# Kernel optimization log

Measured on AMD Instinct MI355X. Metric: run time of the kernel, lower is better.

Reference implementation:

```python
import jax, jax.numpy as jnp
import numpy as np


def _mlp(x, w1, b1, w2, b2):
    # full_connected / full_connected_conv1d with channels [3,16,32]:
    # pointwise Linear -> LeakyReLU -> Linear (kernel-size-1 conv == linear on last dim)
    h = jax.nn.leaky_relu(x @ w1 + b1)
    return h @ w2 + b2


def setup_inputs() -> dict:
    key = jax.random.key(0)
    ks = jax.random.split(key, 10)
    P, K = 100000, 16            # points, neighbors per point
    C_IN, C_H, C_OUT, C_W = 3, 16, 32, 64
    center = jax.random.normal(ks[0], (P, 1, C_IN), dtype=jnp.float32)
    other = jax.random.normal(ks[1], (P, K, C_IN), dtype=jnp.float32)
    s1 = 1.0 / np.sqrt(C_IN)
    s2 = 1.0 / np.sqrt(C_H)
    # 6 stacked 3->16->32 MLPs: [q, center_k, center_v, other_k, other_v, pos]
    mlp_w1 = jax.random.normal(ks[2], (6, C_IN, C_H), dtype=jnp.float32) * s1
    mlp_b1 = jax.random.normal(ks[3], (6, C_H), dtype=jnp.float32) * s1
    mlp_w2 = jax.random.normal(ks[4], (6, C_H, C_OUT), dtype=jnp.float32) * s2
    mlp_b2 = jax.random.normal(ks[5], (6, C_OUT), dtype=jnp.float32) * s2
    # weight_process: 32->64->32
    wp_w1 = jax.random.normal(ks[6], (C_OUT, C_W), dtype=jnp.float32) / np.sqrt(C_OUT)
    wp_b1 = jax.random.normal(ks[7], (C_W,), dtype=jnp.float32) / np.sqrt(C_OUT)
    wp_w2 = jax.random.normal(ks[8], (C_W, C_OUT), dtype=jnp.float32) / np.sqrt(C_W)
    wp_b2 = jax.random.normal(ks[9], (C_OUT,), dtype=jnp.float32) / np.sqrt(C_W)
    return {"center": center, "other": other,
            "mlp_w1": mlp_w1, "mlp_b1": mlp_b1, "mlp_w2": mlp_w2, "mlp_b2": mlp_b2,
            "wp_w1": wp_w1, "wp_b1": wp_b1, "wp_w2": wp_w2, "wp_b2": wp_b2}


def reference(center, other, mlp_w1, mlp_b1, mlp_w2, mlp_b2, wp_w1, wp_b1, wp_w2, wp_b2):
    # center: [P,1,3], other: [P,K,3]
    q = _mlp(center, mlp_w1[0], mlp_b1[0], mlp_w2[0], mlp_b2[0])      # [P,1,32]
    ck = _mlp(center, mlp_w1[1], mlp_b1[1], mlp_w2[1], mlp_b2[1])     # [P,1,32]
    cv = _mlp(center, mlp_w1[2], mlp_b1[2], mlp_w2[2], mlp_b2[2])     # [P,1,32]
    ok = _mlp(other, mlp_w1[3], mlp_b1[3], mlp_w2[3], mlp_b2[3])      # [P,K,32]
    ov = _mlp(other, mlp_w1[4], mlp_b1[4], mlp_w2[4], mlp_b2[4])      # [P,K,32]
    k_all = jnp.concatenate([ck, ok], axis=-2)                        # [P,K+1,32]
    v_all = jnp.concatenate([cv, ov], axis=-2)                        # [P,K+1,32]
    fea_minus = center - jnp.concatenate([center, other], axis=-2)    # [P,K+1,3]
    pos = _mlp(fea_minus, mlp_w1[5], mlp_b1[5], mlp_w2[5], mlp_b2[5]) # [P,K+1,32]
    fea_weight = _mlp(q - k_all + pos, wp_w1, wp_b1, wp_w2, wp_b2)    # [P,K+1,32]
    # vector attention: softmax over CHANNEL dim (-1), weighted sum over neighbors (-2)
    attn = jax.nn.softmax(fea_weight, axis=-1) * (v_all + pos)
    return jnp.sum(attn, axis=-2)                                     # [P,32]
```

## Files before the change

### kernel.cpp

```cpp
#include <hip/hip_runtime.h>


constexpr int PPB = 15;
constexpr float LOG2E = 1.44269504088896340736f;

typedef __attribute__((ext_vector_type(8))) short bf8;
typedef __attribute__((ext_vector_type(4))) float f4;
typedef __attribute__((ext_vector_type(2))) float f2;
typedef __attribute__((ext_vector_type(2))) __bf16 bfp2;

__device__ __forceinline__ unsigned int pkbf(float a, float b) {
  f2 v; v[0] = a; v[1] = b;
  const bfp2 r = __builtin_convertvector(v, bfp2);
  return __builtin_bit_cast(unsigned int, r);
}
__device__ __forceinline__ unsigned short us16(float a) {
  return (unsigned short)((__builtin_bit_cast(unsigned int, a) + 0x8000u) >> 16);
}
__device__ __forceinline__ bf8 mkbf8(const f4& a, const f4& b) {
  uint4 u;
  u.x = pkbf(a[0], a[1]); u.y = pkbf(a[2], a[3]);
  u.z = pkbf(b[0], b[1]); u.w = pkbf(b[2], b[3]);
  return __builtin_bit_cast(bf8, u);
}
__device__ __forceinline__ f4 lrelu4(const f4& v) {
  return __builtin_elementwise_max(v, v * 0.01f);
}
__device__ __forceinline__ f2 lo2(const f4& v) { f2 r; r[0] = v[0]; r[1] = v[1]; return r; }
__device__ __forceinline__ f2 hi2(const f4& v) { f2 r; r[0] = v[2]; r[1] = v[3]; return r; }
__device__ __forceinline__ float exp2appx(float x) {
  const float t = __builtin_fmaf(x, 8388608.0f, 1064992232.0f);
  return __builtin_bit_cast(float, (int)t);
}
__device__ __forceinline__ f4 mfma32(bf8 a, bf8 b, f4 c) {
  return __builtin_amdgcn_mfma_f32_16x16x32_bf16(a, b, c, 0, 0, 0);
}

__device__ __forceinline__ int slotk(int q, int j) {
  return (j < 4) ? (q * 4 + j) : (16 + q * 4 + (j - 4));
}

__device__ __forceinline__ float w1v(const float* mw1, const float* mb1,
                                     int s, int k, int n) {
  const int cb = n >> 4, cc = n & 15;
  const int sk = s ? 1 : 3, sv = s ? 2 : 4;
  if (k < 3)  return cb == 0 ? mw1[sk * 48 + k * 16 + cc]
                   : (cb == 1 ? mw1[sv * 48 + k * 16 + cc] : 0.f);
  if (k < 6)  return cb == 2 ? mw1[5 * 48 + (k - 3) * 16 + cc] : 0.f;
  if (k < 9)  return cb == 3 ? mw1[0 * 48 + (k - 6) * 16 + cc] : 0.f;
  if (k == 9) {
    const int m = (cb == 0) ? sk : (cb == 1) ? sv : (cb == 2) ? 5 : 0;
    return mb1[m * 16 + cc];
  }
  return 0.f;
}
__device__ __forceinline__ float w2v(const float* mw2, int s, int k, int n) {
  const int sk = s ? 1 : 3, sv = s ? 2 : 4;
  if (n < 32) {
    if (k < 16)            return -mw2[sk * 512 + k * 32 + n];
    if (k >= 32 && k < 48) return  mw2[5 * 512 + (k - 32) * 32 + n];
    if (k >= 48)           return  mw2[0 * 512 + (k - 48) * 32 + n];
    return 0.f;
  } else {
    const int cc = n - 32;
    if (k >= 16 && k < 32) return mw2[sv * 512 + (k - 16) * 32 + cc];
    if (k >= 32 && k < 48) return mw2[5 * 512 + (k - 32) * 32 + cc];
    return 0.f;
  }
}

__global__ void prep_kernel(const float* __restrict__ mw1, const float* __restrict__ mb1,
                            const float* __restrict__ mw2, const float* __restrict__ mb2,
                            const float* __restrict__ ww1, const float* __restrict__ ww2,
                            unsigned short* __restrict__ ws16, float* __restrict__ wsf) {
  const int tid = blockIdx.x * 256 + threadIdx.x;
  const int lane = tid & 63, q = lane >> 4, l = lane & 15;
  if (tid < 2048) {
    const int f = tid >> 6;
    for (int j = 0; j < 8; j++) {
      float v;
      if (f < 8) {
        const int s = f >> 2, c = f & 3;
        v = w1v(mw1, mb1, s, q * 8 + j, c * 16 + l);
      } else if (f < 24) {
        const int g = f - 8, s = g >> 3, mc = (g >> 1) & 3, kc2 = g & 1;
        v = w2v(mw2, s, kc2 * 32 + slotk(q, j), mc * 16 + l);
      } else if (f < 28) {
        const int mc = f - 24;
        v = ww1[slotk(q, j) * 64 + mc * 16 + l];
      } else {
        const int g = f - 28, mc2 = g >> 1, kc2 = g & 1;
        v = ww2[(kc2 * 32 + slotk(q, j)) * 32 + mc2 * 16 + l] * LOG2E;
      }
      ws16[f * 512 + lane * 8 + j] = us16(v);
    }
  } else if (tid < 2176) {
    const int t2 = tid - 2048, grp = t2 >> 5, cc = t2 & 31;
    float v;
    if (grp == 0)      v = mb2[cc] - mb2[96 + cc] + mb2[160 + cc];
    else if (grp == 1) v = mb2[128 + cc] + mb2[160 + cc];
    else if (grp == 2) v = mb2[cc] - mb2[32 + cc] + mb2[160 + cc];
    else               v = mb2[64 + cc] + mb2[160 + cc];
    wsf[grp * 32 + cc] = v;
  }
}

__global__ __launch_bounds__(256, 2) void point_attn_kernel(
    const float* __restrict__ center, const float* __restrict__ other,
    const float* __restrict__ wb1, const float* __restrict__ wb2,
    const unsigned short* __restrict__ ws16, const float* __restrict__ wsf,
    float* __restrict__ out, int P) {
  __shared__ float pr[256 * 36];

  const int t = threadIdx.x, lane = t & 63, wv = t >> 6;
  const int q = lane >> 4, l = lane & 15;

  unsigned int d0, d1, d2, d3, d4;
  {
    const int isC = (t >= 240);
    const int pt = isC ? (t - 240) : (t >> 4);
    int p = blockIdx.x * PPB + pt;
    p = p < P ? p : P - 1;
    const float c0 = center[(size_t)p * 3 + 0];
    const float c1 = center[(size_t)p * 3 + 1];
    const float c2 = center[(size_t)p * 3 + 2];
    const float* op = other + ((size_t)p * 16 + (t & 15)) * 3;
    const float o0 = op[0], o1 = op[1], o2 = op[2];
    const float x0 = isC ? c0 : o0, x1 = isC ? c1 : o1, x2 = isC ? c2 : o2;
    const float g0 = c0 - x0, g1 = c1 - x1, g2 = c2 - x2;
    d0 = pkbf(x0, x1); d1 = pkbf(x2, g0); d2 = pkbf(g1, g2);
    d3 = pkbf(c0, c1); d4 = pkbf(c2, 1.0f);
  }

  bf8 W1[4], W2[4][2], P1[4], P2[2][2];
  f4 bw[2], bvp[2], b1f[4], b2f[2];

  auto loadSet = [&](int s) {
#pragma unroll
    for (int c = 0; c < 4; c++)
      W1[c] = *(const bf8*)(ws16 + ((s * 4 + c) * 512 + lane * 8));
#pragma unroll
    for (int mc = 0; mc < 4; mc++)
#pragma unroll
      for (int kc2 = 0; kc2 < 2; kc2++)
        W2[mc][kc2] = *(const bf8*)(ws16 + ((8 + s * 8 + mc * 2 + kc2) * 512 + lane * 8));
#pragma unroll
    for (int mc = 0; mc < 2; mc++) {
      bw[mc]  = *(const f4*)(wsf + s * 64 + mc * 16 + q * 4);
      bvp[mc] = *(const f4*)(wsf + s * 64 + 32 + mc * 16 + q * 4);
    }
  };

  loadSet(wv == 3 ? 1 : 0);
#pragma unroll
  for (int mc = 0; mc < 4; mc++)
    P1[mc] = *(const bf8*)(ws16 + ((24 + mc) * 512 + lane * 8));
#pragma unroll
  for (int mc2 = 0; mc2 < 2; mc2++)
#pragma unroll
    for (int kc2 = 0; kc2 < 2; kc2++)
      P2[mc2][kc2] = *(const bf8*)(ws16 + ((28 + mc2 * 2 + kc2) * 512 + lane * 8));
#pragma unroll
  for (int mc = 0; mc < 4; mc++) b1f[mc] = *(const f4*)(wb1 + mc * 16 + q * 4);
#pragma unroll
  for (int mc2 = 0; mc2 < 2; mc2++) {
    const f4 b = *(const f4*)(wb2 + mc2 * 16 + q * 4);
#pragma unroll
    for (int j = 0; j < 4; j++) b2f[mc2][j] = b[j] * LOG2E;
  }

  auto computeTile = [&](int T) {
    const int src = ((T & 3) << 4) | l;
    const unsigned int s0 = __shfl((int)d0, src), s1 = __shfl((int)d1, src),
                       s2 = __shfl((int)d2, src), s3 = __shfl((int)d3, src),
                       s4 = __shfl((int)d4, src);
    uint4 bu;
    bu.x = q == 0 ? s0 : (q == 1 ? s4 : 0u);
    bu.y = q == 0 ? s1 : 0u;
    bu.z = q == 0 ? s2 : 0u;
    bu.w = q == 0 ? s3 : 0u;
    const bf8 bx = __builtin_bit_cast(bf8, bu);
    const f4 fzero = {0.f, 0.f, 0.f, 0.f};

    f4 D1[4];
#pragma unroll
    for (int c = 0; c < 4; c++)
      D1[c] = lrelu4(mfma32(W1[c], bx, fzero));
    const bf8 hlo = mkbf8(D1[0], D1[1]);
    const bf8 hhi = mkbf8(D1[2], D1[3]);

    f4 wq[2], vpv[2];
#pragma unroll
    for (int mc = 0; mc < 4; mc++) {
      f4 acc = (mc < 2) ? bw[mc] : bvp[mc - 2];
      acc = mfma32(W2[mc][0], hlo, acc);
      acc = mfma32(W2[mc][1], hhi, acc);
      if (mc < 2) wq[mc] = acc; else vpv[mc - 2] = acc;
    }
    const bf8 wB = mkbf8(wq[0], wq[1]);

    f4 h2[4];
#pragma unroll
    for (int mc = 0; mc < 4; mc++)
      h2[mc] = lrelu4(mfma32(P1[mc], wB, b1f[mc]));
    const bf8 h2lo = mkbf8(h2[0], h2[1]);
    const bf8 h2hi = mkbf8(h2[2], h2[3]);

    f4 fw[2];
#pragma unroll
    for (int mc2 = 0; mc2 < 2; mc2++) {
      f4 acc = mfma32(P2[mc2][0], h2lo, b2f[mc2]);
      fw[mc2] = mfma32(P2[mc2][1], h2hi, acc);
    }

    f4 ex0, ex1;
#pragma unroll
    for (int j = 0; j < 4; j++) {
      ex0[j] = exp2appx(fw[0][j]);
      ex1[j] = exp2appx(fw[1][j]);
    }
    const f2 sA = lo2(ex0) + hi2(ex0);
    const f2 sB = lo2(ex1) + hi2(ex1);
    const f2 sC = sA + sB;
    float sum = sC[0] + sC[1];
    sum += __shfl_xor(sum, 16);
    sum += __shfl_xor(sum, 32);
    const float inv = __builtin_amdgcn_rcpf(sum);

    f4 iv; iv[0] = inv; iv[1] = inv; iv[2] = inv; iv[3] = inv;
    const f4 p0 = ex0 * iv * vpv[0];
    const f4 p1 = ex1 * iv * vpv[1];
    *(f4*)&pr[(T * 16 + l) * 36 + q * 4] = p0;
    *(f4*)&pr[(T * 16 + l) * 36 + 16 + q * 4] = p1;
  };

  computeTile(wv == 3 ? 15 : wv * 4);
  if (wv == 3) loadSet(0);
#pragma unroll
  for (int jj = 1; jj < 4; jj++)
    computeTile(wv == 3 ? (11 + jj) : (wv * 4 + jj));

  __syncthreads();

  if (t < 240) {
    const int pp = t >> 4, cp = t & 15;
    f2 s = *(const f2*)&pr[(240 + pp) * 36 + cp * 2];
#pragma unroll
    for (int r2 = 0; r2 < 16; r2++)
      s += *(const f2*)&pr[(pp * 16 + r2) * 36 + cp * 2];
    const int gp = blockIdx.x * PPB + pp;
    if (gp < P) *(f2*)&out[(size_t)gp * 32 + cp * 2] = s;
  }
}

extern "C" void kernel_launch(void* const* d_in, const int* in_sizes, int n_in,
                              void* d_out, int out_size, void* d_ws, size_t ws_size,
                              hipStream_t stream) {
  const float* center = (const float*)d_in[0];
  const float* other  = (const float*)d_in[1];
  unsigned short* ws16 = (unsigned short*)d_ws;
  float* wsf = (float*)((char*)d_ws + 32768);

  prep_kernel<<<9, 256, 0, stream>>>(
      (const float*)d_in[2], (const float*)d_in[3],
      (const float*)d_in[4], (const float*)d_in[5],
      (const float*)d_in[6], (const float*)d_in[8], ws16, wsf);

  const int P = in_sizes[0] / 3;
  const int blocks = (P + PPB - 1) / PPB;
  point_attn_kernel<<<blocks, 256, 0, stream>>>(
      center, other,
      (const float*)d_in[7], (const float*)d_in[9],
      ws16, wsf, (float*)d_out, P);
}
```

Measured before the change: 137.1 us.

## Fold second MLP layer into weight-process first layer to remove an MFMA stage

Because the q−k+pos projection is linear, its second-layer weights are pre-multiplied with the first weight_process layer in the prep kernel. Combined weights and biases (WC, b1p) go into the workspace, so the per-tile wq computation, its bf16 repack and the separate P1 stage are replaced by a K=64 matmul straight from the hidden activations. That removes one dependent MFMA/convert stage per tile. The input shuffles are also hoisted out of the tile loop. Accuracy may shift slightly from folding in fp32 and rounding the combined weights to bf16 once, and the prep kernel grows.

```diff
diff --git a/kernel.cpp b/kernel.cpp
--- a/kernel.cpp
+++ b/kernel.cpp
@@ -72,6 +72,7 @@
 __global__ void prep_kernel(const float* __restrict__ mw1, const float* __restrict__ mb1,
                             const float* __restrict__ mw2, const float* __restrict__ mb2,
                             const float* __restrict__ ww1, const float* __restrict__ ww2,
+                            const float* __restrict__ wb1,
                             unsigned short* __restrict__ ws16, float* __restrict__ wsf) {
   const int tid = blockIdx.x * 256 + threadIdx.x;
   const int lane = tid & 63, q = lane >> 4, l = lane & 15;
@@ -94,8 +95,28 @@
       }
       ws16[f * 512 + lane * 8 + j] = us16(v);
     }
-  } else if (tid < 2176) {
-    const int t2 = tid - 2048, grp = t2 >> 5, cc = t2 & 31;
+  } else if (tid < 3072) {
+    const int g = (tid - 2048) >> 6;
+    const int s = g >> 3, mc = (g >> 1) & 3, kc2 = g & 1;
+    const int m = mc * 16 + l;
+    for (int j = 0; j < 8; j++) {
+      const int k = kc2 * 32 + slotk(q, j);
+      float acc = 0.f;
+      for (int n = 0; n < 32; n++)
+        acc += w2v(mw2, s, k, n) * ww1[n * 64 + m];
+      ws16[(32 + g) * 512 + lane * 8 + j] = us16(acc);
+    }
+  } else if (tid < 3200) {
+    const int t2 = tid - 3072, s = t2 >> 6, m = t2 & 63;
+    float acc = wb1[m];
+    for (int n = 0; n < 32; n++) {
+      const float bwn = s == 0 ? (mb2[n] - mb2[96 + n] + mb2[160 + n])
+                               : (mb2[n] - mb2[32 + n] + mb2[160 + n]);
+      acc += bwn * ww1[n * 64 + m];
+    }
+    wsf[128 + s * 64 + m] = acc;
+  } else if (tid < 3328) {
+    const int t2 = tid - 3200, grp = t2 >> 5, cc = t2 & 31;
     float v;
     if (grp == 0)      v = mb2[cc] - mb2[96 + cc] + mb2[160 + cc];
     else if (grp == 1) v = mb2[128 + cc] + mb2[160 + cc];
@@ -107,7 +128,7 @@
 
 __global__ __launch_bounds__(256, 2) void point_attn_kernel(
     const float* __restrict__ center, const float* __restrict__ other,
-    const float* __restrict__ wb1, const float* __restrict__ wb2,
+    const float* __restrict__ wb2,
     const unsigned short* __restrict__ ws16, const float* __restrict__ wsf,
     float* __restrict__ out, int P) {
   __shared__ float pr[256 * 36];
@@ -132,53 +153,62 @@
     d3 = pkbf(c0, c1); d4 = pkbf(c2, 1.0f);
   }
 
-  bf8 W1[4], W2[4][2], P1[4], P2[2][2];
-  f4 bw[2], bvp[2], b1f[4], b2f[2];
+  uint4 bxr0, bxr1, bxr2, bxr3;
+  {
+    auto gather = [&](int j) {
+      const int src = (j << 4) | l;
+      const unsigned int s0 = __shfl((int)d0, src), s1 = __shfl((int)d1, src),
+                         s2 = __shfl((int)d2, src), s3 = __shfl((int)d3, src),
+                         s4 = __shfl((int)d4, src);
+      uint4 bu;
+      bu.x = q == 0 ? s0 : (q == 1 ? s4 : 0u);
+      bu.y = q == 0 ? s1 : 0u;
+      bu.z = q == 0 ? s2 : 0u;
+      bu.w = q == 0 ? s3 : 0u;
+      return bu;
+    };
+    bxr0 = gather(0); bxr1 = gather(1); bxr2 = gather(2); bxr3 = gather(3);
+  }
+
+  bf8 W1[4], W2v[2][2], WC[4][2], P2[2][2];
+  f4 bvp[2], b1p[4], b2f[2];
 
   auto loadSet = [&](int s) {
 #pragma unroll
     for (int c = 0; c < 4; c++)
       W1[c] = *(const bf8*)(ws16 + ((s * 4 + c) * 512 + lane * 8));
 #pragma unroll
+    for (int mc = 0; mc < 2; mc++)
+#pragma unroll
+      for (int kc2 = 0; kc2 < 2; kc2++)
+        W2v[mc][kc2] = *(const bf8*)(ws16 + ((8 + s * 8 + (mc + 2) * 2 + kc2) * 512 + lane * 8));
+#pragma unroll
     for (int mc = 0; mc < 4; mc++)
 #pragma unroll
       for (int kc2 = 0; kc2 < 2; kc2++)
-        W2[mc][kc2] = *(const bf8*)(ws16 + ((8 + s * 8 + mc * 2 + kc2) * 512 + lane * 8));
-#pragma unroll
-    for (int mc = 0; mc < 2; mc++) {
-      bw[mc]  = *(const f4*)(wsf + s * 64 + mc * 16 + q * 4);
+        WC[mc][kc2] = *(const bf8*)(ws16 + ((32 + s * 8 + mc * 2 + kc2) * 512 + lane * 8));
+#pragma unroll
+    for (int mc = 0; mc < 2; mc++)
       bvp[mc] = *(const f4*)(wsf + s * 64 + 32 + mc * 16 + q * 4);
-    }
+#pragma unroll
+    for (int mc = 0; mc < 4; mc++)
+      b1p[mc] = *(const f4*)(wsf + 128 + s * 64 + mc * 16 + q * 4);
   };
 
   loadSet(wv == 3 ? 1 : 0);
-#pragma unroll
-  for (int mc = 0; mc < 4; mc++)
-    P1[mc] = *(const bf8*)(ws16 + ((24 + mc) * 512 + lane * 8));
 #pragma unroll
   for (int mc2 = 0; mc2 < 2; mc2++)
 #pragma unroll
     for (int kc2 = 0; kc2 < 2; kc2++)
       P2[mc2][kc2] = *(const bf8*)(ws16 + ((28 + mc2 * 2 + kc2) * 512 + lane * 8));
 #pragma unroll
-  for (int mc = 0; mc < 4; mc++) b1f[mc] = *(const f4*)(wb1 + mc * 16 + q * 4);
-#pragma unroll
   for (int mc2 = 0; mc2 < 2; mc2++) {
     const f4 b = *(const f4*)(wb2 + mc2 * 16 + q * 4);
 #pragma unroll
     for (int j = 0; j < 4; j++) b2f[mc2][j] = b[j] * LOG2E;
   }
 
-  auto computeTile = [&](int T) {
-    const int src = ((T & 3) << 4) | l;
-    const unsigned int s0 = __shfl((int)d0, src), s1 = __shfl((int)d1, src),
-                       s2 = __shfl((int)d2, src), s3 = __shfl((int)d3, src),
-                       s4 = __shfl((int)d4, src);
-    uint4 bu;
-    bu.x = q == 0 ? s0 : (q == 1 ? s4 : 0u);
-    bu.y = q == 0 ? s1 : 0u;
-    bu.z = q == 0 ? s2 : 0u;
-    bu.w = q == 0 ? s3 : 0u;
+  auto computeTile = [&](int T, uint4 bu) {
     const bf8 bx = __builtin_bit_cast(bf8, bu);
     const f4 fzero = {0.f, 0.f, 0.f, 0.f};
 
@@ -189,20 +219,20 @@
     const bf8 hlo = mkbf8(D1[0], D1[1]);
     const bf8 hhi = mkbf8(D1[2], D1[3]);
 
-    f4 wq[2], vpv[2];
+    f4 vpv[2];
+#pragma unroll
+    for (int mc = 0; mc < 2; mc++) {
+      f4 acc = mfma32(W2v[mc][0], hlo, bvp[mc]);
+      vpv[mc] = mfma32(W2v[mc][1], hhi, acc);
+    }
+
+    f4 h2[4];
 #pragma unroll
     for (int mc = 0; mc < 4; mc++) {
-      f4 acc = (mc < 2) ? bw[mc] : bvp[mc - 2];
-      acc = mfma32(W2[mc][0], hlo, acc);
-      acc = mfma32(W2[mc][1], hhi, acc);
-      if (mc < 2) wq[mc] = acc; else vpv[mc - 2] = acc;
-    }
-    const bf8 wB = mkbf8(wq[0], wq[1]);
-
-    f4 h2[4];
-#pragma unroll
-    for (int mc = 0; mc < 4; mc++)
-      h2[mc] = lrelu4(mfma32(P1[mc], wB, b1f[mc]));
+      f4 acc = mfma32(WC[mc][1], hhi, b1p[mc]);
+      acc = mfma32(WC[mc][0], hlo, acc);
+      h2[mc] = lrelu4(acc);
+    }
     const bf8 h2lo = mkbf8(h2[0], h2[1]);
     const bf8 h2hi = mkbf8(h2[2], h2[3]);
 
@@ -234,11 +264,14 @@
     *(f4*)&pr[(T * 16 + l) * 36 + 16 + q * 4] = p1;
   };
 
-  computeTile(wv == 3 ? 15 : wv * 4);
-  if (wv == 3) loadSet(0);
-#pragma unroll
-  for (int jj = 1; jj < 4; jj++)
-    computeTile(wv == 3 ? (11 + jj) : (wv * 4 + jj));
+  if (wv == 3) {
+    computeTile(15, bxr3);
+    loadSet(0);
+    computeTile(12, bxr0); computeTile(13, bxr1); computeTile(14, bxr2);
+  } else {
+    computeTile(wv * 4 + 0, bxr0); computeTile(wv * 4 + 1, bxr1);
+    computeTile(wv * 4 + 2, bxr2); computeTile(wv * 4 + 3, bxr3);
+  }
 
   __syncthreads();
 
@@ -259,17 +292,18 @@
   const float* center = (const float*)d_in[0];
   const float* other  = (const float*)d_in[1];
   unsigned short* ws16 = (unsigned short*)d_ws;
-  float* wsf = (float*)((char*)d_ws + 32768);
-
-  prep_kernel<<<9, 256, 0, stream>>>(
+  float* wsf = (float*)((char*)d_ws + 49152);
+
+  prep_kernel<<<13, 256, 0, stream>>>(
       (const float*)d_in[2], (const float*)d_in[3],
       (const float*)d_in[4], (const float*)d_in[5],
-      (const float*)d_in[6], (const float*)d_in[8], ws16, wsf);
+      (const float*)d_in[6], (const float*)d_in[8],
+      (const float*)d_in[7], ws16, wsf);
 
   const int P = in_sizes[0] / 3;
   const int blocks = (P + PPB - 1) / PPB;
   point_attn_kernel<<<blocks, 256, 0, stream>>>(
       center, other,
-      (const float*)d_in[7], (const float*)d_in[9],
+      (const float*)d_in[9],
       ws16, wsf, (float*)d_out, P);
 }
```

Result: slower. 159.2 us (+16.1%).
